# Optimization experiments

Measured on AMD Instinct MI355X. Metric: run time of the kernel, lower is better.

## Reference

```python
import jax, jax.numpy as jnp
import numpy as np
import math

B, N, D, K = 4, 255, 256, 128
NODE_FEATURES_OFFSET = 128
MAX_Z = 101
NUM_EDGES = 2 * NODE_FEATURES_OFFSET + 1  # 257
NUM_DIR_KERNEL = 128  # FourierDirectionalEmbed num_kernel
ECFG_F = 20  # synthetic electron-config feature dim


def setup_inputs() -> dict:
    key = jax.random.key(0)
    ks = jax.random.split(key, 16)
    positions = jax.random.normal(ks[0], (B, N, 3), dtype=jnp.float32) * 3.0
    atomic_numbers = jax.random.randint(ks[1], (B, N), 1, MAX_Z, dtype=jnp.int32)
    s = 0.02
    emb_z = jax.random.normal(ks[2], (MAX_Z + 1, D), dtype=jnp.float32) * s
    electron_config = jax.random.uniform(ks[3], (MAX_Z + 1, ECFG_F), dtype=jnp.float32)
    config_W = jax.random.normal(ks[4], (ECFG_F, D), dtype=jnp.float32) * s
    config_b = jnp.zeros((D,), dtype=jnp.float32)
    mult_W = jax.random.normal(ks[5], (NODE_FEATURES_OFFSET, D), dtype=jnp.float32) * s
    charge_W = jax.random.normal(ks[6], (NODE_FEATURES_OFFSET, D), dtype=jnp.float32) * s
    gbf_means = jax.random.uniform(ks[7], (K,), dtype=jnp.float32, minval=0.0, maxval=7.0)
    gbf_stds = jax.random.uniform(ks[8], (K,), dtype=jnp.float32, minval=0.0, maxval=3.0)
    gbf_mul = jax.random.normal(ks[9], (NUM_EDGES,), dtype=jnp.float32).at[0].set(0.0)  # padding_idx=0
    gbf_bias = (jax.random.normal(ks[10], (NUM_EDGES,), dtype=jnp.float32) * 0.1).at[0].set(0.0)
    proj1_W = jax.random.normal(ks[11], (K, K), dtype=jnp.float32) * (1.0 / math.sqrt(K))
    proj1_b = jnp.zeros((K,), dtype=jnp.float32)
    proj2_W = jax.random.normal(ks[12], (K, D), dtype=jnp.float32) * (1.0 / math.sqrt(K))
    proj2_b = jnp.zeros((D,), dtype=jnp.float32)
    dir_W = jax.random.normal(ks[13], (2 * NUM_DIR_KERNEL, D), dtype=jnp.float32) * (1.0 / math.sqrt(2 * NUM_DIR_KERNEL))
    dir_b = jnp.zeros((D,), dtype=jnp.float32)
    return dict(positions=positions, atomic_numbers=atomic_numbers, emb_z=emb_z,
                electron_config=electron_config, config_W=config_W, config_b=config_b,
                mult_W=mult_W, charge_W=charge_W, gbf_means=gbf_means, gbf_stds=gbf_stds,
                gbf_mul=gbf_mul, gbf_bias=gbf_bias, proj1_W=proj1_W, proj1_b=proj1_b,
                proj2_W=proj2_W, proj2_b=proj2_b, dir_W=dir_W, dir_b=dir_b)


def _angular_freqs():
    min_angle = 1e-4
    half = NUM_DIR_KERNEL // 2
    wl_az = jnp.exp(jnp.linspace(math.log(2 * min_angle), math.log(2 * 2 * math.pi), half))
    wl_po = jnp.exp(jnp.linspace(math.log(2 * min_angle), math.log(2 * math.pi), half))
    return (2 * math.pi / wl_az).astype(jnp.float32), (2 * math.pi / wl_po).astype(jnp.float32)


def _forward(positions, atomic_numbers, emb_z, electron_config, config_W, config_b,
             mult_W, charge_W, gbf_means, gbf_stds, gbf_mul, gbf_bias,
             proj1_W, proj1_b, proj2_W, proj2_b, dir_W, dir_b):
    b = positions.shape[0]
    # add graph-level (CLS) token: zero position, z = MAX_Z = 101
    pos = jnp.concatenate([jnp.zeros_like(positions[:, :1]), positions], axis=1)  # [B,Np,3]
    z = jnp.concatenate([jnp.full_like(atomic_numbers[:, :1], MAX_Z), atomic_numbers], axis=1)  # [B,Np]
    npad = pos.shape[1]

    # --- node embedding: nuclear + electronic + multiplicity(1) + charge(0) ---
    elec = electron_config[z] @ config_W + config_b            # [B,Np,D]
    elec = elec.at[:, 0, :].set(0.0)                            # cls_token row zeroed
    node = emb_z[z] + elec + mult_W[1] + charge_W[0]           # [B,Np,D]

    # --- pairwise geometry: directions[b,i,j] = pos[j] - pos[i] ---
    d = pos[:, None, :, :] - pos[:, :, None, :]                # [B,Np,Np,3]
    sq = jnp.sum(d * d, axis=-1)
    dist = jnp.sqrt(sq + 1e-12)                                # [B,Np,Np]
    nd = d / (dist[..., None] + 1e-5)                          # normed directions, eps per source
    eye = jnp.eye(npad, dtype=bool)[None, :, :]
    x_safe = jnp.where(eye, 1.0, nd[..., 0])
    y_safe = jnp.where(eye, 0.0, nd[..., 1])
    azimuth = jnp.arctan2(y_safe, x_safe)                      # [B,Np,Np]
    polar = jnp.arccos(jnp.clip(nd[..., 2], -1.0 + 1e-6, 1.0 - 1e-6))

    # --- FourierDirectionalEmbed ---
    f_az, f_po = _angular_freqs()
    ph_az = azimuth[..., None] * f_az                          # [B,Np,Np,64]
    ph_po = polar[..., None] * f_po
    sinusoids = jnp.concatenate([jnp.sin(ph_az), jnp.cos(ph_az),
                                 jnp.sin(ph_po), jnp.cos(ph_po)], axis=-1)  # [B,Np,Np,256]
    dir_out = sinusoids @ dir_W + dir_b                        # [B,Np,Np,D]

    # --- Gaussian3DEmbed ---
    zi = z[:, :, None]
    zj = z[:, None, :] + NODE_FEATURES_OFFSET
    mul = gbf_mul[zi] + gbf_mul[zj]                            # sum over the 2 edge-type entries
    bias = gbf_bias[zi] + gbf_bias[zj]                         # [B,Np,Np]
    gx = (mul * dist + bias)[..., None]                        # [B,Np,Np,1] -> broadcast to K
    std = jnp.abs(gbf_stds) + 0.01
    pi_c = 3.14159
    gauss = jnp.exp(-0.5 * ((gx - gbf_means) / std) ** 2) / ((2 * pi_c) ** 0.5 * std)  # [B,Np,Np,K]
    h = jax.nn.gelu(gauss @ proj1_W + proj1_b, approximate=False)
    gbf_out = h @ proj2_W + proj2_b                            # [B,Np,Np,D]

    return node, gbf_out, dir_out


def reference(positions, atomic_numbers, emb_z, electron_config, config_W, config_b,
              mult_W, charge_W, gbf_means, gbf_stds, gbf_mul, gbf_bias,
              proj1_W, proj1_b, proj2_W, proj2_b, dir_W, dir_b):
    return _forward(positions, atomic_numbers, emb_z, electron_config, config_W, config_b,
                    mult_W, charge_W, gbf_means, gbf_stds, gbf_mul, gbf_bias,
                    proj1_W, proj1_b, proj2_W, proj2_b, dir_W, dir_b)
```

## Files before the change

### kernel.cpp

```cpp
#include <hip/hip_runtime.h>
#include <math.h>

typedef __bf16 bf16x8 __attribute__((ext_vector_type(8)));
typedef __bf16 bf16x4 __attribute__((ext_vector_type(4)));
typedef float f32x4 __attribute__((ext_vector_type(4)));
typedef float f32x2 __attribute__((ext_vector_type(2)));

#define PI_D 3.14159265358979323846
#define IH 0.15915494f
#define IL 6.4206383e-9f

__device__ __forceinline__ void bar_lds() {
  __builtin_amdgcn_sched_barrier(0);
  asm volatile("s_waitcnt lgkmcnt(0)" ::: "memory");
  __builtin_amdgcn_s_barrier();
  __builtin_amdgcn_sched_barrier(0);
}

__global__ void setup_kernel(const float* __restrict__ dir_W,
                             const float* __restrict__ proj1_W,
                             const float* __restrict__ proj2_W,
                             const float* __restrict__ gbf_stds,
                             const float* __restrict__ gbf_means,
                             const int* __restrict__ an,
                             const float* __restrict__ emb_z,
                             const float* __restrict__ ec,
                             const float* __restrict__ cW,
                             const float* __restrict__ cb,
                             const float* __restrict__ mult_W,
                             const float* __restrict__ charge_W,
                             __bf16* __restrict__ dirP, __bf16* __restrict__ p1P,
                             __bf16* __restrict__ p2P,
                             float* __restrict__ f_az, float* __restrict__ f_po,
                             f32x2* __restrict__ gAB, float* __restrict__ gcoef,
                             float* __restrict__ out_node) {
  const int bid = blockIdx.x;
  if (bid >= 64) {
    int bi = bid - 64;
    int b = bi >> 8, i = bi & 255;
    int d = threadIdx.x;
    int z = (i == 0) ? 101 : an[b * 255 + i - 1];
    float elec = 0.0f;
    if (i != 0) {
      for (int f = 0; f < 20; ++f) elec += ec[z * 20 + f] * cW[f * 256 + d];
      elec += cb[d];
    }
    float v = emb_z[z * 256 + d] + elec + mult_W[256 + d] + charge_W[d];
    out_node[(size_t)bi * 256 + d] = v;
    return;
  }
  const int tid = threadIdx.x + bid * 256;
  const int nth = 64 * 256;
  for (int o8 = tid; o8 < 8192; o8 += nth) {
    int l = o8 & 63, ks = (o8 >> 6) & 7, nt = o8 >> 9;
    int d = nt * 16 + (l & 15);
    int s0 = ks * 32 + (l >> 4) * 8;
    bf16x8 v;
#pragma unroll
    for (int j = 0; j < 8; ++j) v[j] = (__bf16)dir_W[(s0 + j) * 256 + d];
    *(bf16x8*)(dirP + o8 * 8) = v;
  }
  for (int o8 = tid; o8 < 2048; o8 += nth) {
    int l = o8 & 63, ks = (o8 >> 6) & 3, nt = o8 >> 8;
    int ko = nt * 16 + (l & 15);
    int k0 = ks * 32 + (l >> 4) * 8;
    bf16x8 v;
#pragma unroll
    for (int j = 0; j < 8; ++j) v[j] = (__bf16)proj1_W[(k0 + j) * 128 + ko];
    *(bf16x8*)(p1P + o8 * 8) = v;
  }
  for (int o8 = tid; o8 < 4096; o8 += nth) {
    int l = o8 & 63, ks = (o8 >> 6) & 3, nt = o8 >> 8;
    int d = nt * 16 + (l & 15);
    int k0 = ks * 32 + (l >> 4) * 8;
    bf16x8 v;
#pragma unroll
    for (int j = 0; j < 8; ++j) v[j] = (__bf16)proj2_W[(k0 + j) * 256 + d];
    *(bf16x8*)(p2P + o8 * 8) = v;
  }
  if (bid == 0 && threadIdx.x < 64) {
    int q = threadIdx.x;
    double l0 = log(2.0 * 1e-4);
    double l1a = log(2.0 * 2.0 * PI_D);
    double l1p = log(2.0 * PI_D);
    double ta = l0 + (l1a - l0) * (double)q / 63.0;
    double tp = l0 + (l1p - l0) * (double)q / 63.0;
    f_az[q] = (float)(2.0 * PI_D / exp(ta));
    f_po[q] = (float)(2.0 * PI_D / exp(tp));
  }
  if (bid == 1 && threadIdx.x < 128) {
    int k = threadIdx.x;
    double sd = (double)(fabsf(gbf_stds[k]) + 0.01f);
    double c = sqrt(0.7213475204444817);
    double A = c / sd;
    f32x2 ab;
    ab.x = (float)A;
    ab.y = (float)(-A * (double)gbf_means[k]);
    gAB[k] = ab;
    gcoef[k] = (float)(1.0 / (sqrt(2.0 * 3.14159) * sd));
  }
}

__global__ __launch_bounds__(256, 4) void pair_kernel(
    const float* __restrict__ positions, const int* __restrict__ atomic_numbers,
    const float* __restrict__ gbf_mul, const float* __restrict__ gbf_bias,
    const float* __restrict__ proj1_b, const float* __restrict__ proj2_b,
    const float* __restrict__ dir_b, const __bf16* __restrict__ dirP,
    const __bf16* __restrict__ p1P, const __bf16* __restrict__ p2P,
    const float* __restrict__ f_az, const float* __restrict__ f_po,
    const f32x2* __restrict__ gAB, const float* __restrict__ gcoef,
    float* __restrict__ out_gbf, float* __restrict__ out_dir) {
  __shared__ __align__(16) __bf16 buf[64 * 136];
  __shared__ float s_az[64], s_po[64], s_gx[64];

  const int tid = threadIdx.x;
  const int bid = blockIdx.x;
  const int jt = bid & 3;
  const int i = (bid >> 2) & 255;
  const int b = bid >> 10;
  const int j0 = jt * 64;
  const long pairbase = ((long)(b * 256 + i)) * 256 + j0;

  const int lane = tid & 63, wv = tid >> 6;
  const int lr = lane & 15, kb = lane >> 4;

  const int q8 = (tid & 7) * 8;
  const int pr2 = tid >> 3;
  const int k0g = (tid & 15) * 8;
  const int prow = tid >> 4;

  if (tid < 64) {
    int p = tid, j = j0 + p;
    float pxi = 0.f, pyi = 0.f, pzi = 0.f, pxj = 0.f, pyj = 0.f, pzj = 0.f;
    if (i != 0) { const float* q = positions + ((size_t)b * 255 + (i - 1)) * 3; pxi = q[0]; pyi = q[1]; pzi = q[2]; }
    if (j != 0) { const float* q = positions + ((size_t)b * 255 + (j - 1)) * 3; pxj = q[0]; pyj = q[1]; pzj = q[2]; }
    float dx = pxj - pxi, dy = pyj - pyi, dz = pzj - pzi;
    float sq = dx * dx + dy * dy + dz * dz;
    float dist = sqrtf(sq + 1e-12f);
    float inv = 1.0f / (dist + 1e-5f);
    float ndx = dx * inv, ndy = dy * inv, ndz = dz * inv;
    bool diag = (i == j);
    float xs = diag ? 1.0f : ndx;
    float ys = diag ? 0.0f : ndy;
    s_az[p] = atan2f(ys, xs);
    float cz = fminf(fmaxf(ndz, -1.0f + 1e-6f), 1.0f - 1e-6f);
    s_po[p] = acosf(cz);
    int zi = (i == 0) ? 101 : atomic_numbers[b * 255 + i - 1];
    int zj = ((j == 0) ? 101 : atomic_numbers[b * 255 + j - 1]) + 128;
    float mul = gbf_mul[zi] + gbf_mul[zj];
    float bia = gbf_bias[zi] + gbf_bias[zj];
    s_gx[p] = mul * dist + bia;
  }
  bar_lds();

  f32x4 acc[4][4];
#pragma unroll
  for (int mtl = 0; mtl < 4; ++mtl)
#pragma unroll
    for (int np = 0; np < 4; ++np) acc[mtl][np] = (f32x4){0.f, 0.f, 0.f, 0.f};

  for (int half = 0; half < 2; ++half) {
    const float* ft = half ? f_po : f_az;
    float fv[8];
#pragma unroll
    for (int t = 0; t < 8; ++t) fv[t] = ft[q8 + t];
#pragma unroll
    for (int it = 0; it < 2; ++it) {
      int p = pr2 + it * 32;
      float ang = half ? s_po[p] : s_az[p];
      bf16x8 sv, cv;
#pragma unroll
      for (int t = 0; t < 8; ++t) {
        float ph = ang * fv[t];
        float n = __builtin_rintf(ph * IH);
        float fr = __builtin_fmaf(ph, IH, -n) + ph * IL;
        sv[t] = (__bf16)__builtin_amdgcn_sinf(fr);
        cv[t] = (__bf16)__builtin_amdgcn_cosf(fr);
      }
      *(bf16x8*)(buf + p * 136 + q8) = sv;
      *(bf16x8*)(buf + p * 136 + 64 + q8) = cv;
    }
    bar_lds();
#pragma unroll
    for (int ksl = 0; ksl < 4; ++ksl) {
      int ks = half * 4 + ksl;
      bf16x8 bfr[4];
#pragma unroll
      for (int np = 0; np < 4; ++np)
        bfr[np] = *(const bf16x8*)(buf + (np * 16 + lr) * 136 + ksl * 32 + kb * 8);
#pragma unroll
      for (int mtl = 0; mtl < 4; ++mtl) {
        int mtile = mtl * 4 + wv;
        bf16x8 af = *(const bf16x8*)(dirP + (((size_t)mtile * 8 + ks) * 64 + lane) * 8);
#pragma unroll
        for (int np = 0; np < 4; ++np)
          acc[mtl][np] = __builtin_amdgcn_mfma_f32_16x16x32_bf16(af, bfr[np], acc[mtl][np], 0, 0, 0);
      }
    }
    bar_lds();
  }

  f32x2 abv[8];
  float gcv[8];
#pragma unroll
  for (int t = 0; t < 8; ++t) { abv[t] = gAB[k0g + t]; gcv[t] = gcoef[k0g + t]; }

#pragma unroll
  for (int mtl = 0; mtl < 4; ++mtl) {
    int dcol0 = (mtl * 4 + wv) * 16 + kb * 4;
    f32x4 bias = *(const f32x4*)(dir_b + dcol0);
#pragma unroll
    for (int np = 0; np < 4; ++np) {
      f32x4 v = acc[mtl][np] + bias;
      *(f32x4*)(out_dir + (pairbase + np * 16 + lr) * 256 + dcol0) = v;
    }
  }

#pragma unroll
  for (int it = 0; it < 4; ++it) {
    int p = prow + it * 16;
    float gx = s_gx[p];
    bf16x8 gv;
#pragma unroll
    for (int t = 0; t < 8; ++t) {
      float y = __builtin_fmaf(gx, abv[t].x, abv[t].y);
      gv[t] = (__bf16)(exp2f(-y * y) * gcv[t]);
    }
    *(bf16x8*)(buf + p * 136 + k0g) = gv;
  }
  bar_lds();

  f32x4 acc1[2][4];
#pragma unroll
  for (int mtl = 0; mtl < 2; ++mtl)
#pragma unroll
    for (int np = 0; np < 4; ++np) acc1[mtl][np] = (f32x4){0.f, 0.f, 0.f, 0.f};
#pragma unroll
  for (int ksl = 0; ksl < 4; ++ksl) {
    bf16x8 bfr[4];
#pragma unroll
    for (int np = 0; np < 4; ++np)
      bfr[np] = *(const bf16x8*)(buf + (np * 16 + lr) * 136 + ksl * 32 + kb * 8);
#pragma unroll
    for (int mtl = 0; mtl < 2; ++mtl) {
      int mtile = mtl * 4 + wv;
      bf16x8 af = *(const bf16x8*)(p1P + (((size_t)mtile * 4 + ksl) * 64 + lane) * 8);
#pragma unroll
      for (int np = 0; np < 4; ++np)
        acc1[mtl][np] = __builtin_amdgcn_mfma_f32_16x16x32_bf16(af, bfr[np], acc1[mtl][np], 0, 0, 0);
    }
  }
  bar_lds();

#pragma unroll
  for (int mtl = 0; mtl < 2; ++mtl) {
    int ko0 = (mtl * 4 + wv) * 16 + kb * 4;
    f32x4 pb = *(const f32x4*)(proj1_b + ko0);
#pragma unroll
    for (int np = 0; np < 4; ++np) {
      f32x4 hv = acc1[mtl][np] + pb;
      bf16x4 hb;
#pragma unroll
      for (int r = 0; r < 4; ++r) {
        float v = hv[r];
        v = 0.5f * v * (1.0f + erff(v * 0.70710678118654752f));
        hb[r] = (__bf16)v;
      }
      *(bf16x4*)(buf + (np * 16 + lr) * 136 + ko0) = hb;
    }
  }
  bar_lds();

  f32x4 acc2[4][4];
#pragma unroll
  for (int mtl = 0; mtl < 4; ++mtl)
#pragma unroll
    for (int np = 0; np < 4; ++np) acc2[mtl][np] = (f32x4){0.f, 0.f, 0.f, 0.f};
#pragma unroll
  for (int ksl = 0; ksl < 4; ++ksl) {
    bf16x8 bfr[4];
#pragma unroll
    for (int np = 0; np < 4; ++np)
      bfr[np] = *(const bf16x8*)(buf + (np * 16 + lr) * 136 + ksl * 32 + kb * 8);
#pragma unroll
    for (int mtl = 0; mtl < 4; ++mtl) {
      int mtile = mtl * 4 + wv;
      bf16x8 af = *(const bf16x8*)(p2P + (((size_t)mtile * 4 + ksl) * 64 + lane) * 8);
#pragma unroll
      for (int np = 0; np < 4; ++np)
        acc2[mtl][np] = __builtin_amdgcn_mfma_f32_16x16x32_bf16(af, bfr[np], acc2[mtl][np], 0, 0, 0);
    }
  }
#pragma unroll
  for (int mtl = 0; mtl < 4; ++mtl) {
    int dcol0 = (mtl * 4 + wv) * 16 + kb * 4;
    f32x4 bias = *(const f32x4*)(proj2_b + dcol0);
#pragma unroll
    for (int np = 0; np < 4; ++np) {
      f32x4 v = acc2[mtl][np] + bias;
      *(f32x4*)(out_gbf + (pairbase + np * 16 + lr) * 256 + dcol0) = v;
    }
  }
}

extern "C" void kernel_launch(void* const* d_in, const int* in_sizes, int n_in,
                              void* d_out, int out_size, void* d_ws, size_t ws_size,
                              hipStream_t stream) {
  const float* positions = (const float*)d_in[0];
  const int* atomic_numbers = (const int*)d_in[1];
  const float* emb_z = (const float*)d_in[2];
  const float* electron_config = (const float*)d_in[3];
  const float* config_W = (const float*)d_in[4];
  const float* config_b = (const float*)d_in[5];
  const float* mult_W = (const float*)d_in[6];
  const float* charge_W = (const float*)d_in[7];
  const float* gbf_means = (const float*)d_in[8];
  const float* gbf_stds = (const float*)d_in[9];
  const float* gbf_mul = (const float*)d_in[10];
  const float* gbf_bias = (const float*)d_in[11];
  const float* proj1_W = (const float*)d_in[12];
  const float* proj1_b = (const float*)d_in[13];
  const float* proj2_W = (const float*)d_in[14];
  const float* proj2_b = (const float*)d_in[15];
  const float* dir_W = (const float*)d_in[16];
  const float* dir_b = (const float*)d_in[17];

  float* out = (float*)d_out;
  float* out_node = out;
  float* out_gbf = out + 262144;
  float* out_dir = out + 262144 + 67108864;

  char* ws = (char*)d_ws;
  __bf16* dirP = (__bf16*)(ws);
  __bf16* p1P = (__bf16*)(ws + 131072);
  __bf16* p2P = (__bf16*)(ws + 163840);
  float* f_az = (float*)(ws + 229376);
  float* f_po = (float*)(ws + 229376 + 256);
  f32x2* gAB = (f32x2*)(ws + 229376 + 512);
  float* gcoef = (float*)(ws + 229376 + 1536);

  setup_kernel<<<1088, 256, 0, stream>>>(dir_W, proj1_W, proj2_W, gbf_stds, gbf_means,
                                         atomic_numbers, emb_z, electron_config,
                                         config_W, config_b, mult_W, charge_W,
                                         dirP, p1P, p2P, f_az, f_po, gAB, gcoef,
                                         out_node);
  pair_kernel<<<4096, 256, 0, stream>>>(positions, atomic_numbers, gbf_mul, gbf_bias,
                                        proj1_b, proj2_b, dir_b, dirP, p1P, p2P,
                                        f_az, f_po, gAB, gcoef, out_gbf, out_dir);
}
```

Measured before the change: 164.5 us.

## Split pair kernel into separate directional and Gaussian block types, nontemporal stores

Each 64-pair tile used to be handled by one block that computed both the directional Fourier embedding GEMM and the Gaussian two-layer MLP. The grid is now doubled, and the low bit of the block id chooses which of the two halves a block computes. This shortens each block and lowers per-block register pressure, giving more parallelism to hide latency. It costs some duplicated position and distance computation per tile. Output stores are also switched to nontemporal to avoid polluting the cache on the large write stream.

Result: faster. 147.2 us (-10.5%).

```diff
diff --git a/kernel.cpp b/kernel.cpp
--- a/kernel.cpp
+++ b/kernel.cpp
@@ -111,23 +111,111 @@
     const f32x2* __restrict__ gAB, const float* __restrict__ gcoef,
     float* __restrict__ out_gbf, float* __restrict__ out_dir) {
   __shared__ __align__(16) __bf16 buf[64 * 136];
-  __shared__ float s_az[64], s_po[64], s_gx[64];
+  __shared__ float s_a[64], s_b[64];
 
   const int tid = threadIdx.x;
   const int bid = blockIdx.x;
-  const int jt = bid & 3;
-  const int i = (bid >> 2) & 255;
-  const int b = bid >> 10;
+  const int type = bid & 1;
+  const int tile = bid >> 1;
+  const int jt = tile & 3;
+  const int i = (tile >> 2) & 255;
+  const int b = tile >> 10;
   const int j0 = jt * 64;
   const long pairbase = ((long)(b * 256 + i)) * 256 + j0;
 
   const int lane = tid & 63, wv = tid >> 6;
   const int lr = lane & 15, kb = lane >> 4;
 
-  const int q8 = (tid & 7) * 8;
-  const int pr2 = tid >> 3;
+  if (type == 0) {
+    const int q8 = (tid & 7) * 8;
+    const int pr2 = tid >> 3;
+
+    if (tid < 64) {
+      int p = tid, j = j0 + p;
+      float pxi = 0.f, pyi = 0.f, pzi = 0.f, pxj = 0.f, pyj = 0.f, pzj = 0.f;
+      if (i != 0) { const float* q = positions + ((size_t)b * 255 + (i - 1)) * 3; pxi = q[0]; pyi = q[1]; pzi = q[2]; }
+      if (j != 0) { const float* q = positions + ((size_t)b * 255 + (j - 1)) * 3; pxj = q[0]; pyj = q[1]; pzj = q[2]; }
+      float dx = pxj - pxi, dy = pyj - pyi, dz = pzj - pzi;
+      float sq = dx * dx + dy * dy + dz * dz;
+      float dist = sqrtf(sq + 1e-12f);
+      float inv = 1.0f / (dist + 1e-5f);
+      float ndx = dx * inv, ndy = dy * inv, ndz = dz * inv;
+      bool diag = (i == j);
+      float xs = diag ? 1.0f : ndx;
+      float ys = diag ? 0.0f : ndy;
+      s_a[p] = atan2f(ys, xs);
+      float cz = fminf(fmaxf(ndz, -1.0f + 1e-6f), 1.0f - 1e-6f);
+      s_b[p] = acosf(cz);
+    }
+    bar_lds();
+
+    f32x4 acc[4][4];
+#pragma unroll
+    for (int mtl = 0; mtl < 4; ++mtl)
+#pragma unroll
+      for (int np = 0; np < 4; ++np) acc[mtl][np] = (f32x4){0.f, 0.f, 0.f, 0.f};
+
+    for (int half = 0; half < 2; ++half) {
+      const float* ft = half ? f_po : f_az;
+      float fv[8];
+#pragma unroll
+      for (int t = 0; t < 8; ++t) fv[t] = ft[q8 + t];
+#pragma unroll
+      for (int it = 0; it < 2; ++it) {
+        int p = pr2 + it * 32;
+        float ang = half ? s_b[p] : s_a[p];
+        bf16x8 sv, cv;
+#pragma unroll
+        for (int t = 0; t < 8; ++t) {
+          float ph = ang * fv[t];
+          float n = __builtin_rintf(ph * IH);
+          float fr = __builtin_fmaf(ph, IH, -n) + ph * IL;
+          sv[t] = (__bf16)__builtin_amdgcn_sinf(fr);
+          cv[t] = (__bf16)__builtin_amdgcn_cosf(fr);
+        }
+        *(bf16x8*)(buf + p * 136 + q8) = sv;
+        *(bf16x8*)(buf + p * 136 + 64 + q8) = cv;
+      }
+      bar_lds();
+#pragma unroll
+      for (int ksl = 0; ksl < 4; ++ksl) {
+        int ks = half * 4 + ksl;
+        bf16x8 bfr[4];
+#pragma unroll
+        for (int np = 0; np < 4; ++np)
+          bfr[np] = *(const bf16x8*)(buf + (np * 16 + lr) * 136 + ksl * 32 + kb * 8);
+#pragma unroll
+        for (int mtl = 0; mtl < 4; ++mtl) {
+          int mtile = mtl * 4 + wv;
+          bf16x8 af = *(const bf16x8*)(dirP + (((size_t)mtile * 8 + ks) * 64 + lane) * 8);
+#pragma unroll
+          for (int np = 0; np < 4; ++np)
+            acc[mtl][np] = __builtin_amdgcn_mfma_f32_16x16x32_bf16(af, bfr[np], acc[mtl][np], 0, 0, 0);
+        }
+      }
+      bar_lds();
+    }
+
+#pragma unroll
+    for (int mtl = 0; mtl < 4; ++mtl) {
+      int dcol0 = (mtl * 4 + wv) * 16 + kb * 4;
+      f32x4 bias = *(const f32x4*)(dir_b + dcol0);
+#pragma unroll
+      for (int np = 0; np < 4; ++np) {
+        f32x4 v = acc[mtl][np] + bias;
+        __builtin_nontemporal_store(v, (f32x4*)(out_dir + (pairbase + np * 16 + lr) * 256 + dcol0));
+      }
+    }
+    return;
+  }
+
   const int k0g = (tid & 15) * 8;
   const int prow = tid >> 4;
+
+  f32x2 abv[8];
+  float gcv[8];
+#pragma unroll
+  for (int t = 0; t < 8; ++t) { abv[t] = gAB[k0g + t]; gcv[t] = gcoef[k0g + t]; }
 
   if (tid < 64) {
     int p = tid, j = j0 + p;
@@ -137,89 +225,18 @@
     float dx = pxj - pxi, dy = pyj - pyi, dz = pzj - pzi;
     float sq = dx * dx + dy * dy + dz * dz;
     float dist = sqrtf(sq + 1e-12f);
-    float inv = 1.0f / (dist + 1e-5f);
-    float ndx = dx * inv, ndy = dy * inv, ndz = dz * inv;
-    bool diag = (i == j);
-    float xs = diag ? 1.0f : ndx;
-    float ys = diag ? 0.0f : ndy;
-    s_az[p] = atan2f(ys, xs);
-    float cz = fminf(fmaxf(ndz, -1.0f + 1e-6f), 1.0f - 1e-6f);
-    s_po[p] = acosf(cz);
     int zi = (i == 0) ? 101 : atomic_numbers[b * 255 + i - 1];
     int zj = ((j == 0) ? 101 : atomic_numbers[b * 255 + j - 1]) + 128;
     float mul = gbf_mul[zi] + gbf_mul[zj];
     float bia = gbf_bias[zi] + gbf_bias[zj];
-    s_gx[p] = mul * dist + bia;
+    s_a[p] = mul * dist + bia;
   }
   bar_lds();
-
-  f32x4 acc[4][4];
-#pragma unroll
-  for (int mtl = 0; mtl < 4; ++mtl)
-#pragma unroll
-    for (int np = 0; np < 4; ++np) acc[mtl][np] = (f32x4){0.f, 0.f, 0.f, 0.f};
-
-  for (int half = 0; half < 2; ++half) {
-    const float* ft = half ? f_po : f_az;
-    float fv[8];
-#pragma unroll
-    for (int t = 0; t < 8; ++t) fv[t] = ft[q8 + t];
-#pragma unroll
-    for (int it = 0; it < 2; ++it) {
-      int p = pr2 + it * 32;
-      float ang = half ? s_po[p] : s_az[p];
-      bf16x8 sv, cv;
-#pragma unroll
-      for (int t = 0; t < 8; ++t) {
-        float ph = ang * fv[t];
-        float n = __builtin_rintf(ph * IH);
-        float fr = __builtin_fmaf(ph, IH, -n) + ph * IL;
-        sv[t] = (__bf16)__builtin_amdgcn_sinf(fr);
-        cv[t] = (__bf16)__builtin_amdgcn_cosf(fr);
-      }
-      *(bf16x8*)(buf + p * 136 + q8) = sv;
-      *(bf16x8*)(buf + p * 136 + 64 + q8) = cv;
-    }
-    bar_lds();
-#pragma unroll
-    for (int ksl = 0; ksl < 4; ++ksl) {
-      int ks = half * 4 + ksl;
-      bf16x8 bfr[4];
-#pragma unroll
-      for (int np = 0; np < 4; ++np)
-        bfr[np] = *(const bf16x8*)(buf + (np * 16 + lr) * 136 + ksl * 32 + kb * 8);
-#pragma unroll
-      for (int mtl = 0; mtl < 4; ++mtl) {
-        int mtile = mtl * 4 + wv;
-        bf16x8 af = *(const bf16x8*)(dirP + (((size_t)mtile * 8 + ks) * 64 + lane) * 8);
-#pragma unroll
-        for (int np = 0; np < 4; ++np)
-          acc[mtl][np] = __builtin_amdgcn_mfma_f32_16x16x32_bf16(af, bfr[np], acc[mtl][np], 0, 0, 0);
-      }
-    }
-    bar_lds();
-  }
-
-  f32x2 abv[8];
-  float gcv[8];
-#pragma unroll
-  for (int t = 0; t < 8; ++t) { abv[t] = gAB[k0g + t]; gcv[t] = gcoef[k0g + t]; }
-
-#pragma unroll
-  for (int mtl = 0; mtl < 4; ++mtl) {
-    int dcol0 = (mtl * 4 + wv) * 16 + kb * 4;
-    f32x4 bias = *(const f32x4*)(dir_b + dcol0);
-#pragma unroll
-    for (int np = 0; np < 4; ++np) {
-      f32x4 v = acc[mtl][np] + bias;
-      *(f32x4*)(out_dir + (pairbase + np * 16 + lr) * 256 + dcol0) = v;
-    }
-  }
 
 #pragma unroll
   for (int it = 0; it < 4; ++it) {
     int p = prow + it * 16;
-    float gx = s_gx[p];
+    float gx = s_a[p];
     bf16x8 gv;
 #pragma unroll
     for (int t = 0; t < 8; ++t) {
@@ -298,7 +315,7 @@
 #pragma unroll
     for (int np = 0; np < 4; ++np) {
       f32x4 v = acc2[mtl][np] + bias;
-      *(f32x4*)(out_gbf + (pairbase + np * 16 + lr) * 256 + dcol0) = v;
+      __builtin_nontemporal_store(v, (f32x4*)(out_gbf + (pairbase + np * 16 + lr) * 256 + dcol0));
     }
   }
 }
@@ -344,7 +361,7 @@
                                          config_W, config_b, mult_W, charge_W,
                                          dirP, p1P, p2P, f_az, f_po, gAB, gcoef,
                                          out_node);
-  pair_kernel<<<4096, 256, 0, stream>>>(positions, atomic_numbers, gbf_mul, gbf_bias,
+  pair_kernel<<<8192, 256, 0, stream>>>(positions, atomic_numbers, gbf_mul, gbf_bias,
                                         proj1_b, proj2_b, dir_b, dirP, p1P, p2P,
                                         f_az, f_po, gAB, gcoef, out_gbf, out_dir);
 }
```
